# Performance work log

Hardware: AMD Instinct MI355X
Metric: run time of the kernel (lower is better)

The kernel has to match this reference:

```python
import jax, jax.numpy as jnp
import numpy as np

B, N, D = 8192, 32, 256  # batch, num feature fields, embedding dim


def setup_inputs() -> dict:
    key = jax.random.key(0)
    # x is the stacked feature list: tf.stack(inputs, axis=1) -> [B, N, D]
    x = jax.random.normal(key, (B, N, D), dtype=jnp.float32)
    return {"x": x}


def reference(x):
    """Second-order feature interaction (DLRM dot interaction).

    Computes dot(x_i, x_j) for all field pairs i < j (self_interaction=False),
    flattened in row-major upper-triangular order -> [B, N*(N-1)/2].
    Matches tf.boolean_mask(dot_products, strictly_upper_mask) ordering.
    """
    b, n, d = x.shape
    iu, ju = jnp.triu_indices(n, k=1)          # strictly upper-tri pairs, row-major
    dots = jnp.einsum('bnd,bmd->bnm', x, x)    # [B, N, N] pairwise dot products
    return dots[:, iu, ju]                     # [B, N*(N-1)//2]
```

## Files before the change

kernel.cpp:

```cpp
#include <hip/hip_runtime.h>


constexpr int N_F   = 32;
constexpr int D_EMB = 256;
constexpr int NPAIR = 496;
constexpr int RSTR  = 264;

typedef short  short8 __attribute__((ext_vector_type(8)));
typedef float  f32x4  __attribute__((ext_vector_type(4)));

__device__ __forceinline__ unsigned short f2bf(float f) {
    unsigned int u = __float_as_uint(f);
    u += 0x7FFF + ((u >> 16) & 1);
    return (unsigned short)(u >> 16);
}
__device__ __forceinline__ float bf2f(unsigned short h) {
    return __uint_as_float(((unsigned int)h) << 16);
}

__global__ __launch_bounds__(256, 4)
void soi_mfma(const float* __restrict__ x, float* __restrict__ out) {
    __shared__ unsigned short xhi[N_F * RSTR];
    __shared__ unsigned short xlo[N_F * RSTR];
    __shared__ float sg[N_F * 33];

    const int tid  = threadIdx.x;
    const int b    = blockIdx.x;
    const int lane = tid & 63;
    const int w    = tid >> 6;

    const f32x4* gx = (const f32x4*)(x + (size_t)b * (N_F * D_EMB));
    #pragma unroll
    for (int k = 0; k < 8; ++k) {
        int m   = tid + 256 * k;
        int row = m >> 6;
        int c4  = m & 63;
        f32x4 v = __builtin_nontemporal_load(&gx[m]);
        unsigned short h0 = f2bf(v.x), h1 = f2bf(v.y), h2 = f2bf(v.z), h3 = f2bf(v.w);
        unsigned short l0 = f2bf(v.x - bf2f(h0)), l1 = f2bf(v.y - bf2f(h1)),
                       l2 = f2bf(v.z - bf2f(h2)), l3 = f2bf(v.w - bf2f(h3));
        uint2 hp = make_uint2((unsigned)h0 | ((unsigned)h1 << 16),
                              (unsigned)h2 | ((unsigned)h3 << 16));
        uint2 lp = make_uint2((unsigned)l0 | ((unsigned)l1 << 16),
                              (unsigned)l2 | ((unsigned)l3 << 16));
        *(uint2*)&xhi[row * RSTR + c4 * 4] = hp;
        *(uint2*)&xlo[row * RSTR + c4 * 4] = lp;
    }
    __syncthreads();

    const int wr   = (w >> 1) * 16;
    const int wc   = (w & 1) * 16;
    const int fr   = lane & 15;
    const int quad = lane >> 4;

    const unsigned short* pa_hi = &xhi[(wr + fr) * RSTR + quad * 8];
    const unsigned short* pa_lo = &xlo[(wr + fr) * RSTR + quad * 8];
    const unsigned short* pb_hi = &xhi[(wc + fr) * RSTR + quad * 8];
    const unsigned short* pb_lo = &xlo[(wc + fr) * RSTR + quad * 8];

    f32x4 a1 = {0.f, 0.f, 0.f, 0.f};
    f32x4 a2 = {0.f, 0.f, 0.f, 0.f};
    f32x4 a3 = {0.f, 0.f, 0.f, 0.f};

    #pragma unroll
    for (int s = 0; s < 8; ++s) {
        short8 ahi = *(const short8*)(pa_hi + s * 32);
        short8 alo = *(const short8*)(pa_lo + s * 32);
        short8 bhi = *(const short8*)(pb_hi + s * 32);
        short8 blo = *(const short8*)(pb_lo + s * 32);
        a1 = __builtin_amdgcn_mfma_f32_16x16x32_bf16(ahi, bhi, a1, 0, 0, 0);
        a2 = __builtin_amdgcn_mfma_f32_16x16x32_bf16(ahi, blo, a2, 0, 0, 0);
        a3 = __builtin_amdgcn_mfma_f32_16x16x32_bf16(alo, bhi, a3, 0, 0, 0);
    }

    f32x4 g = a1 + a2 + a3;

    #pragma unroll
    for (int r = 0; r < 4; ++r) {
        int i = wr + quad * 4 + r;
        int j = wc + (lane & 15);
        sg[i * 33 + j] = g[r];
    }
    __syncthreads();

    float* ob = out + (size_t)b * NPAIR;
    #pragma unroll
    for (int k = 0; k < 2; ++k) {
        int p = tid + 256 * k;
        if (p < NPAIR) {
            int i = 0, rem = p;
            while (rem >= N_F - 1 - i) { rem -= N_F - 1 - i; ++i; }
            __builtin_nontemporal_store(sg[i * 33 + i + 1 + rem], &ob[p]);
        }
    }
}

extern "C" void kernel_launch(void* const* d_in, const int* in_sizes, int n_in,
                              void* d_out, int out_size, void* d_ws, size_t ws_size,
                              hipStream_t stream) {
    const float* x = (const float*)d_in[0];
    float* out = (float*)d_out;
    soi_mfma<<<8192, 256, 0, stream>>>(x, out);
}
```

Baseline: 336.4 us.

## Map one batch element per wavefront and feed MFMA straight from registers

Each wavefront now handles one batch element, loading rows directly from global memory into registers and splitting them into bf16 hi/lo parts there, so the LDS staging buffers and the block-wide barriers go away. Only the upper-triangle blocks (00, 01, 11) of the Gram matrix are computed, which skips the redundant 10 block. The split is done by truncation instead of round-to-nearest, and the pair index is computed with a closed form plus correction instead of a serial loop. The cost is four times fewer blocks. The global loads are also strided per lane (each lane reads 32-byte pieces of different rows), which may coalesce worse than the old contiguous loads. Truncating the hi part could also change accuracy slightly.

```diff
diff --git a/kernel.cpp b/kernel.cpp
--- a/kernel.cpp
+++ b/kernel.cpp
@@ -4,93 +4,91 @@
 constexpr int N_F   = 32;
 constexpr int D_EMB = 256;
 constexpr int NPAIR = 496;
-constexpr int RSTR  = 264;
 
-typedef short  short8 __attribute__((ext_vector_type(8)));
-typedef float  f32x4  __attribute__((ext_vector_type(4)));
+typedef short        short8 __attribute__((ext_vector_type(8)));
+typedef float        f32x4  __attribute__((ext_vector_type(4)));
+typedef unsigned int u32x4  __attribute__((ext_vector_type(4)));
 
-__device__ __forceinline__ unsigned short f2bf(float f) {
-    unsigned int u = __float_as_uint(f);
-    u += 0x7FFF + ((u >> 16) & 1);
-    return (unsigned short)(u >> 16);
-}
-__device__ __forceinline__ float bf2f(unsigned short h) {
-    return __uint_as_float(((unsigned int)h) << 16);
+__device__ __forceinline__ void split8(f32x4 A, f32x4 B, short8& hi, short8& lo) {
+    u32x4 au = __builtin_bit_cast(u32x4, A);
+    u32x4 bu = __builtin_bit_cast(u32x4, B);
+    u32x4 ahf = au & 0xFFFF0000u;
+    u32x4 bhf = bu & 0xFFFF0000u;
+    f32x4 la = A - __builtin_bit_cast(f32x4, ahf);
+    f32x4 lb = B - __builtin_bit_cast(f32x4, bhf);
+    u32x4 lau = __builtin_bit_cast(u32x4, la);
+    u32x4 lbu = __builtin_bit_cast(u32x4, lb);
+    u32x4 hp = { (au.x >> 16) | (au.y & 0xFFFF0000u),
+                 (au.z >> 16) | (au.w & 0xFFFF0000u),
+                 (bu.x >> 16) | (bu.y & 0xFFFF0000u),
+                 (bu.z >> 16) | (bu.w & 0xFFFF0000u) };
+    u32x4 lp = { (lau.x >> 16) | (lau.y & 0xFFFF0000u),
+                 (lau.z >> 16) | (lau.w & 0xFFFF0000u),
+                 (lbu.x >> 16) | (lbu.y & 0xFFFF0000u),
+                 (lbu.z >> 16) | (lbu.w & 0xFFFF0000u) };
+    hi = __builtin_bit_cast(short8, hp);
+    lo = __builtin_bit_cast(short8, lp);
 }
 
 __global__ __launch_bounds__(256, 4)
-void soi_mfma(const float* __restrict__ x, float* __restrict__ out) {
-    __shared__ unsigned short xhi[N_F * RSTR];
-    __shared__ unsigned short xlo[N_F * RSTR];
-    __shared__ float sg[N_F * 33];
+void soi_wave(const float* __restrict__ x, float* __restrict__ out) {
+    __shared__ float sg[4][N_F * 33];
 
     const int tid  = threadIdx.x;
-    const int b    = blockIdx.x;
+    const int w    = tid >> 6;
     const int lane = tid & 63;
-    const int w    = tid >> 6;
+    const int fr   = lane & 15;
+    const int q    = lane >> 4;
+    const int b    = (blockIdx.x << 2) + w;
 
-    const f32x4* gx = (const f32x4*)(x + (size_t)b * (N_F * D_EMB));
-    #pragma unroll
-    for (int k = 0; k < 8; ++k) {
-        int m   = tid + 256 * k;
-        int row = m >> 6;
-        int c4  = m & 63;
-        f32x4 v = __builtin_nontemporal_load(&gx[m]);
-        unsigned short h0 = f2bf(v.x), h1 = f2bf(v.y), h2 = f2bf(v.z), h3 = f2bf(v.w);
-        unsigned short l0 = f2bf(v.x - bf2f(h0)), l1 = f2bf(v.y - bf2f(h1)),
-                       l2 = f2bf(v.z - bf2f(h2)), l3 = f2bf(v.w - bf2f(h3));
-        uint2 hp = make_uint2((unsigned)h0 | ((unsigned)h1 << 16),
-                              (unsigned)h2 | ((unsigned)h3 << 16));
-        uint2 lp = make_uint2((unsigned)l0 | ((unsigned)l1 << 16),
-                              (unsigned)l2 | ((unsigned)l3 << 16));
-        *(uint2*)&xhi[row * RSTR + c4 * 4] = hp;
-        *(uint2*)&xlo[row * RSTR + c4 * 4] = lp;
-    }
-    __syncthreads();
+    const float* xb = x + (size_t)b * (N_F * D_EMB);
+    const f32x4* r0 = (const f32x4*)(xb + fr * D_EMB);
+    const f32x4* r1 = (const f32x4*)(xb + (fr + 16) * D_EMB);
 
-    const int wr   = (w >> 1) * 16;
-    const int wc   = (w & 1) * 16;
-    const int fr   = lane & 15;
-    const int quad = lane >> 4;
-
-    const unsigned short* pa_hi = &xhi[(wr + fr) * RSTR + quad * 8];
-    const unsigned short* pa_lo = &xlo[(wr + fr) * RSTR + quad * 8];
-    const unsigned short* pb_hi = &xhi[(wc + fr) * RSTR + quad * 8];
-    const unsigned short* pb_lo = &xlo[(wc + fr) * RSTR + quad * 8];
-
-    f32x4 a1 = {0.f, 0.f, 0.f, 0.f};
-    f32x4 a2 = {0.f, 0.f, 0.f, 0.f};
-    f32x4 a3 = {0.f, 0.f, 0.f, 0.f};
+    f32x4 a00 = {0.f, 0.f, 0.f, 0.f};
+    f32x4 a01 = {0.f, 0.f, 0.f, 0.f};
+    f32x4 a11 = {0.f, 0.f, 0.f, 0.f};
 
     #pragma unroll
     for (int s = 0; s < 8; ++s) {
-        short8 ahi = *(const short8*)(pa_hi + s * 32);
-        short8 alo = *(const short8*)(pa_lo + s * 32);
-        short8 bhi = *(const short8*)(pb_hi + s * 32);
-        short8 blo = *(const short8*)(pb_lo + s * 32);
-        a1 = __builtin_amdgcn_mfma_f32_16x16x32_bf16(ahi, bhi, a1, 0, 0, 0);
-        a2 = __builtin_amdgcn_mfma_f32_16x16x32_bf16(ahi, blo, a2, 0, 0, 0);
-        a3 = __builtin_amdgcn_mfma_f32_16x16x32_bf16(alo, bhi, a3, 0, 0, 0);
+        const int base = s * 8 + q * 2;
+        f32x4 u0 = r0[base];
+        f32x4 u1 = r0[base + 1];
+        f32x4 v0 = r1[base];
+        f32x4 v1 = r1[base + 1];
+        short8 h0, l0, h1, l1;
+        split8(u0, u1, h0, l0);
+        split8(v0, v1, h1, l1);
+        a00 = __builtin_amdgcn_mfma_f32_16x16x32_bf16(h0, h0, a00, 0, 0, 0);
+        a01 = __builtin_amdgcn_mfma_f32_16x16x32_bf16(h0, h1, a01, 0, 0, 0);
+        a11 = __builtin_amdgcn_mfma_f32_16x16x32_bf16(h1, h1, a11, 0, 0, 0);
+        a00 = __builtin_amdgcn_mfma_f32_16x16x32_bf16(h0, l0, a00, 0, 0, 0);
+        a01 = __builtin_amdgcn_mfma_f32_16x16x32_bf16(h0, l1, a01, 0, 0, 0);
+        a11 = __builtin_amdgcn_mfma_f32_16x16x32_bf16(h1, l1, a11, 0, 0, 0);
+        a00 = __builtin_amdgcn_mfma_f32_16x16x32_bf16(l0, h0, a00, 0, 0, 0);
+        a01 = __builtin_amdgcn_mfma_f32_16x16x32_bf16(l0, h1, a01, 0, 0, 0);
+        a11 = __builtin_amdgcn_mfma_f32_16x16x32_bf16(l1, h1, a11, 0, 0, 0);
     }
 
-    f32x4 g = a1 + a2 + a3;
-
+    float* sgw = sg[w];
     #pragma unroll
     for (int r = 0; r < 4; ++r) {
-        int i = wr + quad * 4 + r;
-        int j = wc + (lane & 15);
-        sg[i * 33 + j] = g[r];
+        const int row = q * 4 + r;
+        sgw[row * 33 + fr]             = a00[r];
+        sgw[row * 33 + fr + 16]        = a01[r];
+        sgw[(row + 16) * 33 + fr + 16] = a11[r];
     }
-    __syncthreads();
 
     float* ob = out + (size_t)b * NPAIR;
     #pragma unroll
-    for (int k = 0; k < 2; ++k) {
-        int p = tid + 256 * k;
+    for (int k = 0; k < 8; ++k) {
+        const int p = lane + (k << 6);
         if (p < NPAIR) {
-            int i = 0, rem = p;
-            while (rem >= N_F - 1 - i) { rem -= N_F - 1 - i; ++i; }
-            __builtin_nontemporal_store(sg[i * 33 + i + 1 + rem], &ob[p]);
+            int i = (int)((63.0f - sqrtf(3969.0f - 8.0f * (float)p)) * 0.5f);
+            while (p <  ((i * (63 - i)) >> 1)) --i;
+            while (p >= (((i + 1) * (62 - i)) >> 1)) ++i;
+            const int j = i + 1 + p - ((i * (63 - i)) >> 1);
+            __builtin_nontemporal_store(sgw[i * 33 + j], &ob[p]);
         }
     }
 }
@@ -100,5 +98,5 @@
                               hipStream_t stream) {
     const float* x = (const float*)d_in[0];
     float* out = (float*)d_out;
-    soi_mfma<<<8192, 256, 0, stream>>>(x, out);
+    soi_wave<<<8192 / 4, 256, 0, stream>>>(x, out);
 }
```

New measurement: 365.6 us. 1.09x slower.

## Use single bf16 MFMA pass, skip lower tile, write outputs directly

Applied to the files above, without the earlier changes.

Replaces the hi/lo bf16 split (three MFMAs per step) with a single bf16 product. The wave computing the redundant lower-triangle tile now exits early, and results are stored straight from the accumulators to the packed output, removing the shared Gram buffer and the second barrier. Lower LDS use allows raising the occupancy hint to 8 blocks. The trade is reduced accuracy, since dot products are now computed from bf16-rounded inputs only.

```diff
diff --git a/kernel.cpp b/kernel.cpp
--- a/kernel.cpp
+++ b/kernel.cpp
@@ -9,20 +9,15 @@
 typedef short  short8 __attribute__((ext_vector_type(8)));
 typedef float  f32x4  __attribute__((ext_vector_type(4)));
 
-__device__ __forceinline__ unsigned short f2bf(float f) {
+__device__ __forceinline__ unsigned int f2bf(float f) {
     unsigned int u = __float_as_uint(f);
     u += 0x7FFF + ((u >> 16) & 1);
-    return (unsigned short)(u >> 16);
-}
-__device__ __forceinline__ float bf2f(unsigned short h) {
-    return __uint_as_float(((unsigned int)h) << 16);
+    return u >> 16;
 }
 
-__global__ __launch_bounds__(256, 4)
-void soi_mfma(const float* __restrict__ x, float* __restrict__ out) {
+__global__ __launch_bounds__(256, 8)
+void soi_hi(const float* __restrict__ x, float* __restrict__ out) {
     __shared__ unsigned short xhi[N_F * RSTR];
-    __shared__ unsigned short xlo[N_F * RSTR];
-    __shared__ float sg[N_F * 33];
 
     const int tid  = threadIdx.x;
     const int b    = blockIdx.x;
@@ -36,62 +31,37 @@
         int row = m >> 6;
         int c4  = m & 63;
         f32x4 v = __builtin_nontemporal_load(&gx[m]);
-        unsigned short h0 = f2bf(v.x), h1 = f2bf(v.y), h2 = f2bf(v.z), h3 = f2bf(v.w);
-        unsigned short l0 = f2bf(v.x - bf2f(h0)), l1 = f2bf(v.y - bf2f(h1)),
-                       l2 = f2bf(v.z - bf2f(h2)), l3 = f2bf(v.w - bf2f(h3));
-        uint2 hp = make_uint2((unsigned)h0 | ((unsigned)h1 << 16),
-                              (unsigned)h2 | ((unsigned)h3 << 16));
-        uint2 lp = make_uint2((unsigned)l0 | ((unsigned)l1 << 16),
-                              (unsigned)l2 | ((unsigned)l3 << 16));
+        unsigned int h0 = f2bf(v.x), h1 = f2bf(v.y), h2 = f2bf(v.z), h3 = f2bf(v.w);
+        uint2 hp = make_uint2(h0 | (h1 << 16), h2 | (h3 << 16));
         *(uint2*)&xhi[row * RSTR + c4 * 4] = hp;
-        *(uint2*)&xlo[row * RSTR + c4 * 4] = lp;
     }
     __syncthreads();
 
-    const int wr   = (w >> 1) * 16;
-    const int wc   = (w & 1) * 16;
-    const int fr   = lane & 15;
-    const int quad = lane >> 4;
+    if (w == 2) return;
 
-    const unsigned short* pa_hi = &xhi[(wr + fr) * RSTR + quad * 8];
-    const unsigned short* pa_lo = &xlo[(wr + fr) * RSTR + quad * 8];
-    const unsigned short* pb_hi = &xhi[(wc + fr) * RSTR + quad * 8];
-    const unsigned short* pb_lo = &xlo[(wc + fr) * RSTR + quad * 8];
+    const int fr = lane & 15;
+    const int q  = lane >> 4;
+    const int wr = (w == 3) ? 16 : 0;
+    const int wc = (w == 0) ? 0 : 16;
 
-    f32x4 a1 = {0.f, 0.f, 0.f, 0.f};
-    f32x4 a2 = {0.f, 0.f, 0.f, 0.f};
-    f32x4 a3 = {0.f, 0.f, 0.f, 0.f};
+    const unsigned short* pa = &xhi[(wr + fr) * RSTR + q * 8];
+    const unsigned short* pb = &xhi[(wc + fr) * RSTR + q * 8];
 
+    f32x4 acc = {0.f, 0.f, 0.f, 0.f};
     #pragma unroll
     for (int s = 0; s < 8; ++s) {
-        short8 ahi = *(const short8*)(pa_hi + s * 32);
-        short8 alo = *(const short8*)(pa_lo + s * 32);
-        short8 bhi = *(const short8*)(pb_hi + s * 32);
-        short8 blo = *(const short8*)(pb_lo + s * 32);
-        a1 = __builtin_amdgcn_mfma_f32_16x16x32_bf16(ahi, bhi, a1, 0, 0, 0);
-        a2 = __builtin_amdgcn_mfma_f32_16x16x32_bf16(ahi, blo, a2, 0, 0, 0);
-        a3 = __builtin_amdgcn_mfma_f32_16x16x32_bf16(alo, bhi, a3, 0, 0, 0);
+        short8 af = *(const short8*)(pa + s * 32);
+        short8 bf = *(const short8*)(pb + s * 32);
+        acc = __builtin_amdgcn_mfma_f32_16x16x32_bf16(af, bf, acc, 0, 0, 0);
     }
-
-    f32x4 g = a1 + a2 + a3;
-
-    #pragma unroll
-    for (int r = 0; r < 4; ++r) {
-        int i = wr + quad * 4 + r;
-        int j = wc + (lane & 15);
-        sg[i * 33 + j] = g[r];
-    }
-    __syncthreads();
 
     float* ob = out + (size_t)b * NPAIR;
     #pragma unroll
-    for (int k = 0; k < 2; ++k) {
-        int p = tid + 256 * k;
-        if (p < NPAIR) {
-            int i = 0, rem = p;
-            while (rem >= N_F - 1 - i) { rem -= N_F - 1 - i; ++i; }
-            __builtin_nontemporal_store(sg[i * 33 + i + 1 + rem], &ob[p]);
-        }
+    for (int r = 0; r < 4; ++r) {
+        const int i = wr + q * 4 + r;
+        const int j = wc + fr;
+        if (j > i)
+            ob[((i * (63 - i)) >> 1) + j - i - 1] = acc[r];
     }
 }
 
@@ -100,5 +70,5 @@
                               hipStream_t stream) {
     const float* x = (const float*)d_in[0];
     float* out = (float*)d_out;
-    soi_mfma<<<8192, 256, 0, stream>>>(x, out);
+    soi_hi<<<8192, 256, 0, stream>>>(x, out);
 }
```

Measured after the change: 337.1 us. Within noise of the previous version (+0.2%).
